# Kernel tuning notes

Measured on AMD Instinct MI355X. Metric: run time of the kernel, lower is better.

Reference implementation:

```python
import jax, jax.numpy as jnp
import numpy as np

B, CIN, CE, CA, N, S = 2, 64, 128, 128, 1024, 32
SCALE = np.sqrt(np.float32(CA))  # scale_mode == 'dimfts'


def _vnlin(W, x):
    # VNLinear: linear map over the channel dim of (B, C, 3, N, S)
    return jnp.einsum('oc,bcdns->bodns', W, x)


def setup_inputs() -> dict:
    key = jax.random.key(0)
    ks = jax.random.split(key, 16)
    def w(k, o, i):
        return (jax.random.normal(k, (o, i), jnp.float32) / np.sqrt(np.float32(i)))
    return {
        'group_xyz': jax.random.normal(ks[0], (B, N, S, 3), jnp.float32),
        'group_fts': jax.random.normal(ks[1], (B, CIN, 3, N, S), jnp.float32),
        'query_xyz': jax.random.normal(ks[2], (B, N, 3), jnp.float32),
        'W_e1': w(ks[3], CE, CIN), 'W_e2': w(ks[4], CE, CE),
        'W_q': w(ks[5], CA, CE), 'W_k': w(ks[6], CA, CE), 'W_v': w(ks[7], CA, CE),
        'W_r1': w(ks[8], 64, 1), 'W_r2': w(ks[9], CA, 64),
        'W_std': w(ks[10], 3, CA),
        'W_f1': w(ks[11], CA, CA * 3), 'b_f1': jax.random.normal(ks[12], (CA,), jnp.float32) * 0.02,
        'W_f2': w(ks[13], CA, CA), 'b_f2': jax.random.normal(ks[14], (CA,), jnp.float32) * 0.02,
    }


def reference(group_xyz, group_fts, query_xyz, W_e1, W_e2, W_q, W_k, W_v,
              W_r1, W_r2, W_std, W_f1, b_f1, W_f2, b_f2):
    # vnn_e: two stacked VNLinear layers
    group_emb = _vnlin(W_e2, _vnlin(W_e1, group_fts))        # (B, CE, 3, N, S)
    query_emb = group_emb[..., :1]                           # (B, CE, 3, N, 1)
    q = _vnlin(W_q, query_emb)                               # (B, CA, 3, N, 1)
    k = _vnlin(W_k, group_emb)                               # (B, CA, 3, N, S)
    v = _vnlin(W_v, group_emb)                               # (B, CA, 3, N, S)

    # positional relation: xyz_rel -> (B, 1, 3, N, S) -> vnn_r
    xyz_rel = group_xyz - query_xyz[:, :, None, :]           # (B, N, S, 3)
    xyz_rel = jnp.transpose(xyz_rel[:, :, :, None, :], (0, 3, 4, 1, 2))  # (B,1,3,N,S)
    pos_rel = _vnlin(W_r2, _vnlin(W_r1, xyz_rel))            # (B, CA, 3, N, S)

    # relation_func == 'sub'
    attn = q - k + pos_rel                                   # (B, CA, 3, N, S)

    # VNStdFeatureLin (dim=5, no frame normalization): z0 = VNLinear(CA->3)
    z0 = _vnlin(W_std, attn)                                 # (B, 3, 3, N, S)
    attn = jnp.einsum('bijns,bjkns->bikns', attn, z0)        # (B, CA, 3, N, S) invariant

    # attn_fwd: 1x1 conv -> ReLU -> 1x1 conv on (B, CA*3, N, S)
    attn = attn.reshape(B, CA * 3, N, S)
    h = jax.nn.relu(jnp.einsum('oc,bcns->bons', W_f1, attn) + b_f1[:, None, None])
    a = jnp.einsum('oc,bcns->bons', W_f2, h) + b_f2[:, None, None]  # (B, CA, N, S)

    a = jax.nn.softmax(a[:, :, None, :, :] / SCALE, axis=-1)  # (B, CA, 1, N, S)
    v = v + pos_rel
    resi = jnp.sum(a * v, axis=-1)                            # (B, CA, 3, N)
    return resi
```

## Files before the change

kernel.cpp:

```cpp
#include <hip/hip_runtime.h>
#include <hip/hip_bf16.h>
#include <math.h>

typedef __hip_bfloat16  bf16;
typedef __hip_bfloat162 bf162;
typedef __attribute__((ext_vector_type(8))) short short8;
typedef __attribute__((ext_vector_type(4))) float f32x4;

#define BB   2
#define CINC 64
#define NN   1024
#define SSS  32
#define NS   (NN * SSS)

#define OFF_WE21 0
#define OFF_WR   8192
#define OFF_KBA  8320
#define OFF_VB   16512
#define OFF_F1B  20608
#define OFF_F2B  45184
#define WS_NEED_FLOATS 53376

#define S_ATT_B  0
#define S_FTS_B  26112
#define S_SCR_B  26112
#define S_QSRC_B 33024
#define S_XYZ_B  33184
#define SMEM_BYTES 33408

__device__ __forceinline__ float bf2f(short s) {
    unsigned int u = ((unsigned int)(unsigned short)s) << 16;
    return __uint_as_float(u);
}
__device__ __forceinline__ short f2bf(float f) {
    bf16 h = __float2bfloat16(f);
    return *reinterpret_cast<short*>(&h);
}
__device__ __forceinline__ unsigned pk2(float a, float b) {
    bf162 p = __float22bfloat162_rn(make_float2(a, b));
    return *reinterpret_cast<unsigned*>(&p);
}

__global__ __launch_bounds__(256) void prep1(const float* __restrict__ We1,
                                             const float* __restrict__ We2,
                                             float* __restrict__ ws) {
    int e = blockIdx.x * 256 + threadIdx.x;
    int o = e >> 6, c = e & 63;
    float acc = 0.f;
    for (int m = 0; m < 128; ++m)
        acc = fmaf(We2[o * 128 + m], We1[m * 64 + c], acc);
    ws[OFF_WE21 + o * 64 + c] = acc;
}

__global__ __launch_bounds__(256) void prep2(const float* __restrict__ Wq,
                                             const float* __restrict__ Wk,
                                             const float* __restrict__ Wv,
                                             const float* __restrict__ Wr1,
                                             const float* __restrict__ Wr2,
                                             const float* __restrict__ Wf1,
                                             const float* __restrict__ Wf2,
                                             float* __restrict__ ws) {
    const float* we21 = ws + OFF_WE21;
    int e = blockIdx.x * 256 + threadIdx.x;
    if (e < 16384) {
        int i = e >> 7, c2 = e & 127;
        const float* W = (c2 < 64) ? Wk : Wq;
        int c = c2 & 63;
        float acc = 0.f;
        for (int o = 0; o < 128; ++o)
            acc = fmaf(W[i * 128 + o], we21[o * 64 + c], acc);
        if (c2 >= 64) acc = -acc;
        ((bf16*)(ws + OFF_KBA))[i * 128 + c2] = __float2bfloat16(acc);
    } else if (e < 24576) {
        int le = e - 16384;
        int i = le >> 6, c = le & 63;
        float acc = 0.f;
        for (int o = 0; o < 128; ++o)
            acc = fmaf(Wv[i * 128 + o], we21[o * 64 + c], acc);
        ((bf16*)(ws + OFF_VB))[i * 64 + c] = __float2bfloat16(acc);
    } else if (e < 24704) {
        int i = e - 24576;
        float acc = 0.f;
        for (int m = 0; m < 64; ++m)
            acc = fmaf(Wr2[i * 64 + m], Wr1[m], acc);
        ws[OFF_WR + i] = acc;
    } else if (e < 24704 + 49152) {
        int f = e - 24704;
        int o = f / 384, kp = f - o * 384;
        int c = (kp & 127) * 3 + (kp >> 7);
        ((bf16*)(ws + OFF_F1B))[f] = __float2bfloat16(Wf1[o * 384 + c]);
    } else if (e < 24704 + 49152 + 16384) {
        int f = e - (24704 + 49152);
        ((bf16*)(ws + OFF_F2B))[f] = __float2bfloat16(Wf2[f]);
    }
}

__global__ __launch_bounds__(256, 2) void fused_main(
        const float* __restrict__ gxyz, const float* __restrict__ gfts,
        const float* __restrict__ qxyz, const float* __restrict__ Wstd,
        const float* __restrict__ bf1,  const float* __restrict__ bf2,
        const float* __restrict__ ws,   float* __restrict__ out) {
    extern __shared__ char smc[];
    short* s_att  = (short*)(smc + S_ATT_B);
    short* h_t    = s_att;
    short* a_t    = s_att + 4352;
    short* fts_s  = (short*)(smc + S_FTS_B);
    float* s_scr  = (float*)(smc + S_SCR_B);
    short* q_src  = (short*)(smc + S_QSRC_B);
    short* s_xyzh = (short*)(smc + S_XYZ_B);

    const int t    = threadIdx.x;
    const int bid  = blockIdx.x;
    const int b    = bid >> 10;
    const int n    = bid & 1023;
    const int w    = t >> 6;
    const int lane = t & 63;
    const int quad = lane >> 4;
    const int lq   = lane & 15;
    const int wb   = 32 * w;

    const float* gb = gfts + (size_t)b * (CINC * 3 * NS) + n * SSS;

    short8 Ka[2][4], Va[2][2];
    {
        const short* kba = (const short*)(ws + OFF_KBA);
        const short* vbb = (const short*)(ws + OFF_VB);
        #pragma unroll
        for (int it = 0; it < 2; ++it) {
            int i = wb + it * 16 + lq;
            #pragma unroll
            for (int kc = 0; kc < 4; ++kc)
                Ka[it][kc] = *(const short8*)(kba + i * 128 + kc * 32 + quad * 8);
            #pragma unroll
            for (int kc = 0; kc < 2; ++kc)
                Va[it][kc] = *(const short8*)(vbb + i * 64 + kc * 32 + quad * 8);
        }
    }
    float wr2[2] = { ws[OFF_WR + wb + lq], ws[OFF_WR + wb + 16 + lq] };

    uint2 va_pk[6][2];
    #pragma unroll
    for (int h = 0; h < 2; ++h) {
        for (int l4 = t; l4 < 768; l4 += 256) {
            int c  = l4 / 12;
            int mq = l4 - c * 12;
            int ml = mq * 4;
            int mg = h * 48 + ml;
            int d  = mg >> 5, s = mg & 31;
            float4 f = *(const float4*)(gb + (c * 3 + d) * NS + s);
            fts_s[(ml + 0) * 72 + c] = f2bf(f.x);
            fts_s[(ml + 1) * 72 + c] = f2bf(f.y);
            fts_s[(ml + 2) * 72 + c] = f2bf(f.z);
            fts_s[(ml + 3) * 72 + c] = f2bf(f.w);
            if (h == 0 && ml == 32) q_src[c] = f2bf(f.x);
        }
        if (h == 0 && t >= 160) {
            int id = t - 160;
            int d = id >> 5, s = id & 31;
            s_xyzh[id] = f2bf(gxyz[((b * NN + n) * SSS + s) * 3 + d]
                              - qxyz[(b * NN + n) * 3 + d]);
        }
        __syncthreads();

        #pragma unroll
        for (int mt_h = 0; mt_h < 3; ++mt_h) {
            int mt = h * 3 + mt_h;
            int d  = mt >> 1;
            const short* ap = fts_s + (mt_h * 16 + lq) * 72 + quad * 8;
            short8 a0 = *(const short8*)(ap);
            short8 a1 = *(const short8*)(ap + 32);
            const short* qp;
            if (h == 0) qp = fts_s + (d * 32) * 72 + quad * 8;
            else        qp = (d == 1) ? (q_src + quad * 8)
                                      : (fts_s + 16 * 72 + quad * 8);
            short8 aq0 = *(const short8*)(qp);
            short8 aq1 = *(const short8*)(qp + 32);
            #pragma unroll
            for (int it = 0; it < 2; ++it) {
                f32x4 kk = {0.f, 0.f, 0.f, 0.f};
                kk = __builtin_amdgcn_mfma_f32_16x16x32_bf16(a0,  Ka[it][0], kk, 0, 0, 0);
                kk = __builtin_amdgcn_mfma_f32_16x16x32_bf16(a1,  Ka[it][1], kk, 0, 0, 0);
                kk = __builtin_amdgcn_mfma_f32_16x16x32_bf16(aq0, Ka[it][2], kk, 0, 0, 0);
                kk = __builtin_amdgcn_mfma_f32_16x16x32_bf16(aq1, Ka[it][3], kk, 0, 0, 0);
                f32x4 vv = {0.f, 0.f, 0.f, 0.f};
                vv = __builtin_amdgcn_mfma_f32_16x16x32_bf16(a0,  Va[it][0], vv, 0, 0, 0);
                vv = __builtin_amdgcn_mfma_f32_16x16x32_bf16(a1,  Va[it][1], vv, 0, 0, 0);
                int i = wb + it * 16 + lq;
                float p[4];
                #pragma unroll
                for (int reg = 0; reg < 4; ++reg) {
                    int m = mt * 16 + quad * 4 + reg;
                    float pos = wr2[it] * bf2f(s_xyzh[m]);
                    s_att[m * 136 + i] = f2bf(pos - kk[reg]);
                    p[reg] = vv[reg] + pos;
                }
                va_pk[mt][it].x = pk2(p[0], p[1]);
                va_pk[mt][it].y = pk2(p[2], p[3]);
            }
        }
        __syncthreads();
    }

    {
        short8 As[4];
        #pragma unroll
        for (int kc = 0; kc < 4; ++kc) {
            short8 a = {0, 0, 0, 0, 0, 0, 0, 0};
            if (lq < 3) {
                const float* wp = Wstd + lq * 128 + kc * 32 + quad * 8;
                float4 w0 = *(const float4*)(wp);
                float4 w1 = *(const float4*)(wp + 4);
                a[0] = f2bf(w0.x); a[1] = f2bf(w0.y); a[2] = f2bf(w0.z); a[3] = f2bf(w0.w);
                a[4] = f2bf(w1.x); a[5] = f2bf(w1.y); a[6] = f2bf(w1.z); a[7] = f2bf(w1.w);
            }
            As[kc] = a;
        }
        for (int tile = w; tile < 6; tile += 4) {
            f32x4 acc = {0.f, 0.f, 0.f, 0.f};
            const short* bp = s_att + (tile * 16 + lq) * 136 + quad * 8;
            #pragma unroll
            for (int kc = 0; kc < 4; ++kc) {
                short8 bfr = *(const short8*)(bp + kc * 32);
                acc = __builtin_amdgcn_mfma_f32_16x16x32_bf16(As[kc], bfr, acc, 0, 0, 0);
            }
            if (quad == 0) {
                #pragma unroll
                for (int reg = 0; reg < 3; ++reg)
                    s_scr[reg * 96 + tile * 16 + lq] = acc[reg];
            }
        }
    }
    __syncthreads();

    for (int u = t; u < 512; u += 256) {
        int s  = u >> 4;
        int i0 = (u & 15) * 8;
        float z[3][3];
        #pragma unroll
        for (int j = 0; j < 3; ++j)
            #pragma unroll
            for (int kk = 0; kk < 3; ++kk)
                z[j][kk] = s_scr[j * 96 + kk * 32 + s];
        float af[3][8];
        #pragma unroll
        for (int j = 0; j < 3; ++j) {
            short8 v8 = *(const short8*)(s_att + (j * 32 + s) * 136 + i0);
            #pragma unroll
            for (int x = 0; x < 8; ++x) af[j][x] = bf2f(v8[x]);
        }
        #pragma unroll
        for (int kk = 0; kk < 3; ++kk) {
            short8 o8;
            #pragma unroll
            for (int x = 0; x < 8; ++x)
                o8[x] = f2bf(af[0][x] * z[0][kk] + af[1][x] * z[1][kk] + af[2][x] * z[2][kk]);
            *(short8*)(s_att + (kk * 32 + s) * 136 + i0) = o8;
        }
    }
    __syncthreads();

    f32x4 eacc[2][2];
    {
        f32x4 zz = {0.f, 0.f, 0.f, 0.f};
        eacc[0][0] = zz; eacc[0][1] = zz; eacc[1][0] = zz; eacc[1][1] = zz;
        const short* f1b = (const short*)(ws + OFF_F1B);
        const short* ab0 = f1b + (wb + lq) * 384 + quad * 8;
        const short* ab1 = ab0 + 16 * 384;
        #pragma unroll 2
        for (int ks = 0; ks < 12; ++ks) {
            int kk = ks >> 2;
            int ic = (ks & 3) * 32 + quad * 8;
            short8 a0 = *(const short8*)(ab0 + ks * 32);
            short8 a1 = *(const short8*)(ab1 + ks * 32);
            const short* bp = s_att + (kk * 32) * 136 + ic;
            short8 b0 = *(const short8*)(bp + lq * 136);
            short8 b1 = *(const short8*)(bp + (lq + 16) * 136);
            eacc[0][0] = __builtin_amdgcn_mfma_f32_16x16x32_bf16(a0, b0, eacc[0][0], 0, 0, 0);
            eacc[0][1] = __builtin_amdgcn_mfma_f32_16x16x32_bf16(a0, b1, eacc[0][1], 0, 0, 0);
            eacc[1][0] = __builtin_amdgcn_mfma_f32_16x16x32_bf16(a1, b0, eacc[1][0], 0, 0, 0);
            eacc[1][1] = __builtin_amdgcn_mfma_f32_16x16x32_bf16(a1, b1, eacc[1][1], 0, 0, 0);
        }
    }
    __syncthreads();

    #pragma unroll
    for (int mt = 0; mt < 2; ++mt) {
        int ob = wb + mt * 16 + quad * 4;
        float4 bb = *(const float4*)(bf1 + ob);
        float bv[4] = {bb.x, bb.y, bb.z, bb.w};
        #pragma unroll
        for (int nt = 0; nt < 2; ++nt) {
            f32x4 c = eacc[mt][nt];
            int s = nt * 16 + lq;
            uint2 pk;
            pk.x = pk2(fmaxf(c[0] + bv[0], 0.f), fmaxf(c[1] + bv[1], 0.f));
            pk.y = pk2(fmaxf(c[2] + bv[2], 0.f), fmaxf(c[3] + bv[3], 0.f));
            *(uint2*)(h_t + s * 136 + ob) = pk;
        }
    }
    __syncthreads();

    {
        f32x4 facc[2][2];
        f32x4 zz = {0.f, 0.f, 0.f, 0.f};
        facc[0][0] = zz; facc[0][1] = zz; facc[1][0] = zz; facc[1][1] = zz;
        const short* f2b = (const short*)(ws + OFF_F2B);
        const short* ab0 = f2b + (wb + lq) * 128 + quad * 8;
        const short* ab1 = ab0 + 16 * 128;
        #pragma unroll 2
        for (int ks = 0; ks < 4; ++ks) {
            int c0 = ks * 32 + quad * 8;
            short8 a0 = *(const short8*)(ab0 + ks * 32);
            short8 a1 = *(const short8*)(ab1 + ks * 32);
            short8 b0 = *(const short8*)(h_t + lq * 136 + c0);
            short8 b1 = *(const short8*)(h_t + (lq + 16) * 136 + c0);
            facc[0][0] = __builtin_amdgcn_mfma_f32_16x16x32_bf16(a0, b0, facc[0][0], 0, 0, 0);
            facc[0][1] = __builtin_amdgcn_mfma_f32_16x16x32_bf16(a0, b1, facc[0][1], 0, 0, 0);
            facc[1][0] = __builtin_amdgcn_mfma_f32_16x16x32_bf16(a1, b0, facc[1][0], 0, 0, 0);
            facc[1][1] = __builtin_amdgcn_mfma_f32_16x16x32_bf16(a1, b1, facc[1][1], 0, 0, 0);
        }
        #pragma unroll
        for (int mt = 0; mt < 2; ++mt) {
            int ob = wb + mt * 16 + quad * 4;
            float4 bb = *(const float4*)(bf2 + ob);
            float bv[4] = {bb.x, bb.y, bb.z, bb.w};
            #pragma unroll
            for (int nt = 0; nt < 2; ++nt) {
                f32x4 c = facc[mt][nt];
                int s = nt * 16 + lq;
                uint2 pk;
                pk.x = pk2(c[0] + bv[0], c[1] + bv[1]);
                pk.y = pk2(c[2] + bv[2], c[3] + bv[3]);
                *(uint2*)(a_t + s * 136 + ob) = pk;
            }
        }
    }
    __syncthreads();

    if (t < 128) {
        float vals[32];
        #pragma unroll
        for (int s = 0; s < 32; ++s) vals[s] = bf2f(a_t[s * 136 + t]);
        float mx = -INFINITY;
        #pragma unroll
        for (int s = 0; s < 32; ++s) mx = fmaxf(mx, vals[s]);
        const float inv = 0.08838834764831845f;
        float sum = 0.f;
        #pragma unroll
        for (int s = 0; s < 32; ++s) { vals[s] = __expf((vals[s] - mx) * inv); sum += vals[s]; }
        float rs = 1.f / sum;
        #pragma unroll
        for (int s = 0; s < 32; ++s) a_t[s * 136 + t] = f2bf(vals[s] * rs);
    }
    __syncthreads();

    {
        float pr[2][3];
        #pragma unroll
        for (int it = 0; it < 2; ++it)
            #pragma unroll
            for (int d = 0; d < 3; ++d) pr[it][d] = 0.f;
        #pragma unroll
        for (int mt = 0; mt < 6; ++mt) {
            int d = mt >> 1;
            int s0 = (mt & 1) * 16 + quad * 4;
            #pragma unroll
            for (int it = 0; it < 2; ++it) {
                int i = wb + it * 16 + lq;
                uint2 vp = va_pk[mt][it];
                float v0 = bf2f((short)(vp.x & 0xffff));
                float v1 = bf2f((short)(vp.x >> 16));
                float v2 = bf2f((short)(vp.y & 0xffff));
                float v3 = bf2f((short)(vp.y >> 16));
                pr[it][d] = fmaf(bf2f(a_t[(s0 + 0) * 136 + i]), v0, pr[it][d]);
                pr[it][d] = fmaf(bf2f(a_t[(s0 + 1) * 136 + i]), v1, pr[it][d]);
                pr[it][d] = fmaf(bf2f(a_t[(s0 + 2) * 136 + i]), v2, pr[it][d]);
                pr[it][d] = fmaf(bf2f(a_t[(s0 + 3) * 136 + i]), v3, pr[it][d]);
            }
        }
        #pragma unroll
        for (int it = 0; it < 2; ++it)
            #pragma unroll
            for (int d = 0; d < 3; ++d) {
                float v = pr[it][d];
                v += __shfl_xor(v, 16);
                v += __shfl_xor(v, 32);
                if (quad == 0) s_scr[(wb + it * 16 + lq) * 3 + d] = v;
            }
    }
    __syncthreads();

    for (int e = t; e < 384; e += 256)
        out[(b * 384 + e) * NN + n] = s_scr[e];
}

extern "C" void kernel_launch(void* const* d_in, const int* in_sizes, int n_in,
                              void* d_out, int out_size, void* d_ws, size_t ws_size,
                              hipStream_t stream) {
    const float* gxyz = (const float*)d_in[0];
    const float* gfts = (const float*)d_in[1];
    const float* qxyz = (const float*)d_in[2];
    const float* We1  = (const float*)d_in[3];
    const float* We2  = (const float*)d_in[4];
    const float* Wq   = (const float*)d_in[5];
    const float* Wk   = (const float*)d_in[6];
    const float* Wv   = (const float*)d_in[7];
    const float* Wr1  = (const float*)d_in[8];
    const float* Wr2  = (const float*)d_in[9];
    const float* Wstd = (const float*)d_in[10];
    const float* bf1  = (const float*)d_in[12];
    const float* bf2  = (const float*)d_in[14];
    float* out = (float*)d_out;
    float* ws  = (float*)d_ws;

    (void)hipFuncSetAttribute((const void*)fused_main,
                              hipFuncAttributeMaxDynamicSharedMemorySize, SMEM_BYTES);

    prep1<<<32, 256, 0, stream>>>(We1, We2, ws);
    prep2<<<353, 256, 0, stream>>>(Wq, Wk, Wv, Wr1, Wr2,
                                   (const float*)d_in[11], (const float*)d_in[13], ws);
    fused_main<<<BB * NN, 256, SMEM_BYTES, stream>>>(gxyz, gfts, qxyz, Wstd,
                                                     bf1, bf2, ws, out);
}
```

Before: 189.5 us.

## Restage feature loads per spatial dim and fuse softmax into GEMM epilogue

```diff
diff --git a/kernel.cpp b/kernel.cpp
--- a/kernel.cpp
+++ b/kernel.cpp
@@ -24,9 +24,8 @@
 #define S_ATT_B  0
 #define S_FTS_B  26112
 #define S_SCR_B  26112
-#define S_QSRC_B 33024
-#define S_XYZ_B  33184
-#define SMEM_BYTES 33408
+#define S_XYZ_B  30720
+#define SMEM_BYTES 30912
 
 __device__ __forceinline__ float bf2f(short s) {
     unsigned int u = ((unsigned int)(unsigned short)s) << 16;
@@ -106,7 +105,6 @@
     short* a_t    = s_att + 4352;
     short* fts_s  = (short*)(smc + S_FTS_B);
     float* s_scr  = (float*)(smc + S_SCR_B);
-    short* q_src  = (short*)(smc + S_QSRC_B);
     short* s_xyzh = (short*)(smc + S_XYZ_B);
 
     const int t    = threadIdx.x;
@@ -140,19 +138,18 @@
 
     uint2 va_pk[6][2];
     #pragma unroll
-    for (int h = 0; h < 2; ++h) {
-        for (int l4 = t; l4 < 768; l4 += 256) {
-            int c  = l4 / 12;
-            int mq = l4 - c * 12;
-            int ml = mq * 4;
-            int mg = h * 48 + ml;
-            int d  = mg >> 5, s = mg & 31;
-            float4 f = *(const float4*)(gb + (c * 3 + d) * NS + s);
-            fts_s[(ml + 0) * 72 + c] = f2bf(f.x);
-            fts_s[(ml + 1) * 72 + c] = f2bf(f.y);
-            fts_s[(ml + 2) * 72 + c] = f2bf(f.z);
-            fts_s[(ml + 3) * 72 + c] = f2bf(f.w);
-            if (h == 0 && ml == 32) q_src[c] = f2bf(f.x);
+    for (int h = 0; h < 3; ++h) {
+        {
+            int cp = t >> 3;
+            int ml = (t & 7) * 4;
+            const float* fb = gb + (2 * cp * 3 + h) * NS + ml;
+            float4 f0 = *(const float4*)(fb);
+            float4 f1 = *(const float4*)(fb + 3 * NS);
+            short* dst = fts_s + ml * 72 + 2 * cp;
+            *(unsigned*)(dst)       = pk2(f0.x, f1.x);
+            *(unsigned*)(dst + 72)  = pk2(f0.y, f1.y);
+            *(unsigned*)(dst + 144) = pk2(f0.z, f1.z);
+            *(unsigned*)(dst + 216) = pk2(f0.w, f1.w);
         }
         if (h == 0 && t >= 160) {
             int id = t - 160;
@@ -162,19 +159,15 @@
         }
         __syncthreads();
 
-        #pragma unroll
-        for (int mt_h = 0; mt_h < 3; ++mt_h) {
-            int mt = h * 3 + mt_h;
-            int d  = mt >> 1;
+        const short* qp = fts_s + quad * 8;
+        short8 aq0 = *(const short8*)(qp);
+        short8 aq1 = *(const short8*)(qp + 32);
+        #pragma unroll
+        for (int mt_h = 0; mt_h < 2; ++mt_h) {
+            int mt = h * 2 + mt_h;
             const short* ap = fts_s + (mt_h * 16 + lq) * 72 + quad * 8;
             short8 a0 = *(const short8*)(ap);
             short8 a1 = *(const short8*)(ap + 32);
-            const short* qp;
-            if (h == 0) qp = fts_s + (d * 32) * 72 + quad * 8;
-            else        qp = (d == 1) ? (q_src + quad * 8)
-                                      : (fts_s + 16 * 72 + quad * 8);
-            short8 aq0 = *(const short8*)(qp);
-            short8 aq1 = *(const short8*)(qp + 32);
             #pragma unroll
             for (int it = 0; it < 2; ++it) {
                 f32x4 kk = {0.f, 0.f, 0.f, 0.f};
@@ -319,38 +312,41 @@
             facc[1][0] = __builtin_amdgcn_mfma_f32_16x16x32_bf16(a1, b0, facc[1][0], 0, 0, 0);
             facc[1][1] = __builtin_amdgcn_mfma_f32_16x16x32_bf16(a1, b1, facc[1][1], 0, 0, 0);
         }
+        const float inv = 0.08838834764831845f;
         #pragma unroll
         for (int mt = 0; mt < 2; ++mt) {
             int ob = wb + mt * 16 + quad * 4;
             float4 bb = *(const float4*)(bf2 + ob);
             float bv[4] = {bb.x, bb.y, bb.z, bb.w};
-            #pragma unroll
-            for (int nt = 0; nt < 2; ++nt) {
-                f32x4 c = facc[mt][nt];
-                int s = nt * 16 + lq;
-                uint2 pk;
-                pk.x = pk2(c[0] + bv[0], c[1] + bv[1]);
-                pk.y = pk2(c[2] + bv[2], c[3] + bv[3]);
-                *(uint2*)(a_t + s * 136 + ob) = pk;
-            }
-        }
-    }
-    __syncthreads();
-
-    if (t < 128) {
-        float vals[32];
-        #pragma unroll
-        for (int s = 0; s < 32; ++s) vals[s] = bf2f(a_t[s * 136 + t]);
-        float mx = -INFINITY;
-        #pragma unroll
-        for (int s = 0; s < 32; ++s) mx = fmaxf(mx, vals[s]);
-        const float inv = 0.08838834764831845f;
-        float sum = 0.f;
-        #pragma unroll
-        for (int s = 0; s < 32; ++s) { vals[s] = __expf((vals[s] - mx) * inv); sum += vals[s]; }
-        float rs = 1.f / sum;
-        #pragma unroll
-        for (int s = 0; s < 32; ++s) a_t[s * 136 + t] = f2bf(vals[s] * rs);
+            float a0v[4], a1v[4];
+            #pragma unroll
+            for (int reg = 0; reg < 4; ++reg) {
+                float v0 = facc[mt][0][reg] + bv[reg];
+                float v1 = facc[mt][1][reg] + bv[reg];
+                float mx = fmaxf(v0, v1);
+                mx = fmaxf(mx, __shfl_xor(mx, 1));
+                mx = fmaxf(mx, __shfl_xor(mx, 2));
+                mx = fmaxf(mx, __shfl_xor(mx, 4));
+                mx = fmaxf(mx, __shfl_xor(mx, 8));
+                float e0 = __expf((v0 - mx) * inv);
+                float e1 = __expf((v1 - mx) * inv);
+                float sm = e0 + e1;
+                sm += __shfl_xor(sm, 1);
+                sm += __shfl_xor(sm, 2);
+                sm += __shfl_xor(sm, 4);
+                sm += __shfl_xor(sm, 8);
+                float rs = 1.f / sm;
+                a0v[reg] = e0 * rs;
+                a1v[reg] = e1 * rs;
+            }
+            uint2 pk;
+            pk.x = pk2(a0v[0], a0v[1]);
+            pk.y = pk2(a0v[2], a0v[3]);
+            *(uint2*)(a_t + lq * 136 + ob) = pk;
+            pk.x = pk2(a1v[0], a1v[1]);
+            pk.y = pk2(a1v[2], a1v[3]);
+            *(uint2*)(a_t + (16 + lq) * 136 + ob) = pk;
+        }
     }
     __syncthreads();
 
```

Result: faster. 184.6 us (-2.6%).
